# Kernel optimization log

Hardware: AMD Instinct MI355X
Metric: run time of the kernel (lower is better)

The kernel has to match this reference:

```python
import jax, jax.numpy as jnp
import numpy as np

B, S, L, H = 8, 4, 512, 768
N_SPANS, T_MAX = 4096, 16
N_PAIRS = 16384


def setup_inputs() -> dict:
    key = jax.random.key(0)
    k1, k2, k3, k4, k5, k6 = jax.random.split(key, 6)
    hidden = jax.random.normal(k1, (B, S, L, H), dtype=jnp.float32)
    span_doc = jax.random.randint(k2, (N_SPANS,), 0, B, dtype=jnp.int32)
    # per-span padded, sorted subtoken indices into the flattened S*L window axis
    span_tok = jnp.sort(jax.random.randint(k3, (N_SPANS, T_MAX), 0, S * L, dtype=jnp.int32), axis=1)
    span_len = jax.random.randint(k4, (N_SPANS,), 1, T_MAX + 1, dtype=jnp.int32)
    pair_i = jax.random.randint(k5, (N_PAIRS,), 0, N_SPANS, dtype=jnp.int32)
    pair_j = jax.random.randint(k6, (N_PAIRS,), 0, N_SPANS, dtype=jnp.int32)
    return {"hidden": hidden, "span_doc": span_doc, "span_tok": span_tok,
            "span_len": span_len, "pair_i": pair_i, "pair_j": pair_j}


def reference(hidden, span_doc, span_tok, span_len, pair_i, pair_j):
    # hidden: [B, S, L, H]; flatten windows so span_tok indexes S*L directly
    b, s, l, h = hidden.shape
    hf = hidden.reshape(b, s * l, h)
    # ragged gather: [N, T, H]
    g = hf[span_doc[:, None], span_tok]
    n, t = span_tok.shape
    mask = (jnp.arange(t, dtype=jnp.int32)[None, :] < span_len[:, None])  # [N, T]
    denom = span_len.astype(hidden.dtype)[:, None]
    mean = jnp.sum(g * mask[..., None].astype(hidden.dtype), axis=1) / denom  # [N, H]
    first = g[:, 0]                                      # first subtoken of span
    last = g[jnp.arange(n), span_len - 1]                # last valid subtoken
    reprs = jnp.concatenate([first, mean, last], axis=-1)  # [N, 3H]
    pairs = jnp.concatenate([reprs[pair_i], reprs[pair_j]], axis=-1)  # [P, 6H]
    return pairs
```

## Files before the change

### kernel.cpp

```cpp
#include <hip/hip_runtime.h>


#define SPAN_H    768
#define SPAN_HF4  192
#define SPAN_TMAX 16
#define SPAN_SL   2048

__global__ __launch_bounds__(192)
void span_pooler_40097814675703_kernel(
    const float4* __restrict__ hidden,
    const int*    __restrict__ span_doc,
    const int*    __restrict__ span_tok,
    const int*    __restrict__ span_len,
    const int*    __restrict__ pair_i,
    const int*    __restrict__ pair_j,
    float4*       __restrict__ out)
{
    const int p = blockIdx.x;
    const int c = threadIdx.x;

    const int si = pair_i[p];
    const int sj = pair_j[p];

    float4* orow = out + (size_t)p * 1152;

    #pragma unroll
    for (int side = 0; side < 2; ++side) {
        const int s   = side ? sj : si;
        const int doc = span_doc[s];
        const int len = span_len[s];
        const int* toks = span_tok + s * SPAN_TMAX;
        const float4* base = hidden + (size_t)doc * (SPAN_SL * SPAN_HF4);

        float4 first = make_float4(0.f, 0.f, 0.f, 0.f);
        float4 last  = make_float4(0.f, 0.f, 0.f, 0.f);
        float sx = 0.f, sy = 0.f, sz = 0.f, sw = 0.f;

        for (int t = 0; t < len; ++t) {
            const float4 v = base[(size_t)toks[t] * SPAN_HF4 + c];
            if (t == 0) first = v;
            last = v;
            sx += v.x; sy += v.y; sz += v.z; sw += v.w;
        }

        const float inv = 1.0f / (float)len;
        const float4 mean = make_float4(sx * inv, sy * inv, sz * inv, sw * inv);

        float4* o = orow + side * 576;
        o[c]       = first;
        o[192 + c] = mean;
        o[384 + c] = last;
    }
}

extern "C" void kernel_launch(void* const* d_in, const int* in_sizes, int n_in,
                              void* d_out, int out_size, void* d_ws, size_t ws_size,
                              hipStream_t stream) {
    const float4* hidden  = (const float4*)d_in[0];
    const int* span_doc   = (const int*)d_in[1];
    const int* span_tok   = (const int*)d_in[2];
    const int* span_len   = (const int*)d_in[3];
    const int* pair_i     = (const int*)d_in[4];
    const int* pair_j     = (const int*)d_in[5];
    float4* out           = (float4*)d_out;

    const int n_pairs = in_sizes[4];

    span_pooler_40097814675703_kernel<<<n_pairs, 192, 0, stream>>>(
        hidden, span_doc, span_tok, span_len, pair_i, pair_j, out);
}
```

Measured before the change: 424.1 us.

## Compute span representations once into workspace, then gather them into pairs

Splits the work into two kernels. The first pools each span once (first, mean, last) into a workspace buffer, and the second gathers those rows into the pair output with a grid-stride loop. Each span is no longer re-gathered from hidden for every pair that references it. The token loop is also fully unrolled to T_MAX with clamped indices and masked accumulation, so loads can issue in parallel but padded tokens are now loaded redundantly. The fused kernel remains as a fallback when the workspace is too small.

```diff
diff --git a/kernel.cpp b/kernel.cpp
--- a/kernel.cpp
+++ b/kernel.cpp
@@ -1,13 +1,82 @@
 #include <hip/hip_runtime.h>
 
 
-#define SPAN_H    768
 #define SPAN_HF4  192
 #define SPAN_TMAX 16
 #define SPAN_SL   2048
+#define REPR_F4   576
+#define OUT_F4    1152
 
 __global__ __launch_bounds__(192)
-void span_pooler_40097814675703_kernel(
+void span_reprs_kernel(
+    const float4* __restrict__ hidden,
+    const int*    __restrict__ span_doc,
+    const int*    __restrict__ span_tok,
+    const int*    __restrict__ span_len,
+    float4*       __restrict__ reprs)
+{
+    const int s = blockIdx.x;
+    const int c = threadIdx.x;
+
+    const int doc = span_doc[s];
+    const int len = span_len[s];
+    const int* toks = span_tok + s * SPAN_TMAX;
+    const float4* base = hidden + (size_t)doc * (SPAN_SL * SPAN_HF4);
+
+    float4 first = make_float4(0.f, 0.f, 0.f, 0.f);
+    float4 last  = make_float4(0.f, 0.f, 0.f, 0.f);
+    float sx = 0.f, sy = 0.f, sz = 0.f, sw = 0.f;
+
+    #pragma unroll
+    for (int t = 0; t < SPAN_TMAX; ++t) {
+        const int tc = (t < len) ? t : (len - 1);
+        const float4 v = base[(size_t)toks[tc] * SPAN_HF4 + c];
+        if (t == 0) first = v;
+        last = v;
+        const float m = (t < len) ? 1.f : 0.f;
+        sx += v.x * m; sy += v.y * m; sz += v.z * m; sw += v.w * m;
+    }
+
+    const float inv = 1.0f / (float)len;
+    float4* r = reprs + (size_t)s * REPR_F4;
+    r[c]       = first;
+    r[SPAN_HF4 + c] = make_float4(sx * inv, sy * inv, sz * inv, sw * inv);
+    r[2 * SPAN_HF4 + c] = last;
+}
+
+__global__ __launch_bounds__(192)
+void span_pairs_kernel(
+    const float4* __restrict__ reprs,
+    const int*    __restrict__ pair_i,
+    const int*    __restrict__ pair_j,
+    float4*       __restrict__ out,
+    int n_pairs)
+{
+    const int c = threadIdx.x;
+    for (int p = blockIdx.x; p < n_pairs; p += gridDim.x) {
+        const int pi = pair_i[p];
+        const int pj = pair_j[p];
+        const float4* ri = reprs + (size_t)pi * REPR_F4;
+        const float4* rj = reprs + (size_t)pj * REPR_F4;
+        float4* o = out + (size_t)p * OUT_F4;
+
+        const float4 a0 = ri[c];
+        const float4 a1 = ri[SPAN_HF4 + c];
+        const float4 a2 = ri[2 * SPAN_HF4 + c];
+        const float4 b0 = rj[c];
+        const float4 b1 = rj[SPAN_HF4 + c];
+        const float4 b2 = rj[2 * SPAN_HF4 + c];
+        o[c]                 = a0;
+        o[SPAN_HF4 + c]      = a1;
+        o[2 * SPAN_HF4 + c]  = a2;
+        o[3 * SPAN_HF4 + c]  = b0;
+        o[4 * SPAN_HF4 + c]  = b1;
+        o[5 * SPAN_HF4 + c]  = b2;
+    }
+}
+
+__global__ __launch_bounds__(192)
+void span_fused_kernel(
     const float4* __restrict__ hidden,
     const int*    __restrict__ span_doc,
     const int*    __restrict__ span_tok,
@@ -18,11 +87,9 @@
 {
     const int p = blockIdx.x;
     const int c = threadIdx.x;
-
     const int si = pair_i[p];
     const int sj = pair_j[p];
-
-    float4* orow = out + (size_t)p * 1152;
+    float4* orow = out + (size_t)p * OUT_F4;
 
     #pragma unroll
     for (int side = 0; side < 2; ++side) {
@@ -35,21 +102,20 @@
         float4 first = make_float4(0.f, 0.f, 0.f, 0.f);
         float4 last  = make_float4(0.f, 0.f, 0.f, 0.f);
         float sx = 0.f, sy = 0.f, sz = 0.f, sw = 0.f;
-
-        for (int t = 0; t < len; ++t) {
-            const float4 v = base[(size_t)toks[t] * SPAN_HF4 + c];
+        #pragma unroll
+        for (int t = 0; t < SPAN_TMAX; ++t) {
+            const int tc = (t < len) ? t : (len - 1);
+            const float4 v = base[(size_t)toks[tc] * SPAN_HF4 + c];
             if (t == 0) first = v;
             last = v;
-            sx += v.x; sy += v.y; sz += v.z; sw += v.w;
+            const float m = (t < len) ? 1.f : 0.f;
+            sx += v.x * m; sy += v.y * m; sz += v.z * m; sw += v.w * m;
         }
-
         const float inv = 1.0f / (float)len;
-        const float4 mean = make_float4(sx * inv, sy * inv, sz * inv, sw * inv);
-
-        float4* o = orow + side * 576;
-        o[c]       = first;
-        o[192 + c] = mean;
-        o[384 + c] = last;
+        float4* o = orow + side * REPR_F4;
+        o[c]                = first;
+        o[SPAN_HF4 + c]     = make_float4(sx * inv, sy * inv, sz * inv, sw * inv);
+        o[2 * SPAN_HF4 + c] = last;
     }
 }
 
@@ -64,8 +130,18 @@
     const int* pair_j     = (const int*)d_in[5];
     float4* out           = (float4*)d_out;
 
+    const int n_spans = in_sizes[1];
     const int n_pairs = in_sizes[4];
+    const size_t reprs_bytes = (size_t)n_spans * REPR_F4 * sizeof(float4);
 
-    span_pooler_40097814675703_kernel<<<n_pairs, 192, 0, stream>>>(
-        hidden, span_doc, span_tok, span_len, pair_i, pair_j, out);
+    if (ws_size >= reprs_bytes) {
+        float4* reprs = (float4*)d_ws;
+        span_reprs_kernel<<<n_spans, 192, 0, stream>>>(
+            hidden, span_doc, span_tok, span_len, reprs);
+        span_pairs_kernel<<<4096, 192, 0, stream>>>(
+            reprs, pair_i, pair_j, out, n_pairs);
+    } else {
+        span_fused_kernel<<<n_pairs, 192, 0, stream>>>(
+            hidden, span_doc, span_tok, span_len, pair_i, pair_j, out);
+    }
 }
```

New measurement: 390.6 us. 7.9% less time.
